# Performance work log

Hardware: AMD Instinct MI355X
Metric: run time of the kernel (lower is better)

## Reference

```python
import jax, jax.numpy as jnp
import numpy as np

C = 768
N = 2048
BS = 8
MASK_VAL = 1e10


def _sincos(n, c):
    # torch sinusoidal_position_embedding: interleaved sin/cos, then
    # cos_pos = emb[..., 1::2].repeat_interleave(2), sin_pos = emb[..., ::2].repeat_interleave(2)
    pos = jnp.arange(n, dtype=jnp.float32)[:, None]            # [N,1]
    inv = jnp.power(10000.0, -2.0 * jnp.arange(c // 2, dtype=jnp.float32) / c)  # [C/2]
    ang = pos * inv                                            # [N, C/2]
    sin = jnp.repeat(jnp.sin(ang), 2, axis=-1)                 # [N, C]
    cos = jnp.repeat(jnp.cos(ang), 2, axis=-1)                 # [N, C]
    return sin[None], cos[None]                                # [1, N, C]


def _rope(x, sin, cos):
    # x2 = interleave(-x_odd, x_even)
    x2 = jnp.stack([-x[..., 1::2], x[..., ::2]], axis=-1).reshape(x.shape)
    return x * cos + x2 * sin


def _global_pointer(x, Wq, bq, Wk, bk, sin, cos, mask):
    xq = jnp.einsum('bnc,dc->bnd', x, Wq) + bq
    xk = jnp.einsum('bnc,dc->bnd', x, Wk) + bk
    xq = _rope(xq, sin, cos)
    xk = _rope(xk, sin, cos)
    logits = jnp.einsum('bnd,bmd->bnm', xq, xk)
    logits = logits - mask * MASK_VAL
    return logits / jnp.sqrt(jnp.float32(C))


def setup_inputs() -> dict:
    key = jax.random.key(0)
    ks = jax.random.split(key, 9)
    s = 0.02
    return {
        'feature': jax.random.normal(ks[0], (BS, N, C), jnp.float32),
        'Wq': jax.random.normal(ks[1], (C, C), jnp.float32) * s,
        'bq': jax.random.normal(ks[2], (C,), jnp.float32) * s,
        'Wk': jax.random.normal(ks[3], (C, C), jnp.float32) * s,
        'bk': jax.random.normal(ks[4], (C,), jnp.float32) * s,
        'Wq_cls': jax.random.normal(ks[5], (C, C), jnp.float32) * s,
        'bq_cls': jax.random.normal(ks[6], (C,), jnp.float32) * s,
        'Wk_cls': jax.random.normal(ks[7], (C, C), jnp.float32) * s,
        'bk_cls': jax.random.normal(ks[8], (C,), jnp.float32) * s,
    }


def reference(feature, Wq, bq, Wk, bk, Wq_cls, bq_cls, Wk_cls, bk_cls):
    n = feature.shape[1]
    sin, cos = _sincos(n, C)
    mask = jnp.tril(jnp.ones((n, n), jnp.float32), k=-1)  # strictly lower triangular
    gp = _global_pointer(feature, Wq, bq, Wk, bk, sin, cos, mask)
    gp_cls = _global_pointer(feature, Wq_cls, bq_cls, Wk_cls, bk_cls, sin, cos, mask)
    # stacked: [2, bs, N, N] = (global_pointer, global_pointer_cls)
    return jnp.stack([gp, gp_cls], axis=0)
```

## Files before the change

kernel.cpp:

```cpp
#include <hip/hip_runtime.h>
#include <hip/hip_bf16.h>
#include <stdint.h>

typedef unsigned short u16;
typedef __attribute__((ext_vector_type(8))) __bf16 bf16x8;
typedef __attribute__((ext_vector_type(4))) float f32x4;

#define C_DIM 768
#define HALF_C 384
#define N_SEQ 2048
#define BATCH 8
#define M_TOT (BATCH * N_SEQ)
#define BK 32
#define NT (C_DIM / BK)

__device__ __forceinline__ u16 f2bf(float f) {
    union { float f; unsigned u; } c; c.f = f;
    unsigned r = (c.u + 0x7FFFu + ((c.u >> 16) & 1u)) >> 16;
    return (u16)r;
}

#define NXF4   3145728
#define NWF4   147456
#define NCONV4 (NXF4 + 4 * NWF4)
#define NCS    (N_SEQ * HALF_C)
__global__ __launch_bounds__(256) void prep_kernel(
    const float* __restrict__ feat,
    const float* __restrict__ Wq, const float* __restrict__ Wk,
    const float* __restrict__ Wqc, const float* __restrict__ Wkc,
    u16* __restrict__ xbf,
    u16* __restrict__ w0, u16* __restrict__ w1,
    u16* __restrict__ w2, u16* __restrict__ w3,
    uint32_t* __restrict__ cs_tab) {
    const int gid = blockIdx.x * 256 + threadIdx.x;
    const int stride = gridDim.x * 256;
    for (int i = gid; i < NCONV4; i += stride) {
        const float* src; u16* dst; int j;
        if (i < NXF4) { src = feat; dst = xbf; j = i; }
        else {
            const int k = i - NXF4;
            const int w = k / NWF4;
            j = k - w * NWF4;
            src = w == 0 ? Wq : w == 1 ? Wk : w == 2 ? Wqc : Wkc;
            dst = w == 0 ? w0 : w == 1 ? w1 : w == 2 ? w2 : w3;
        }
        float4 v = ((const float4*)src)[j];
        ushort4 o;
        o.x = f2bf(v.x); o.y = f2bf(v.y); o.z = f2bf(v.z); o.w = f2bf(v.w);
        ((ushort4*)dst)[j] = o;
    }
    for (int idx = gid; idx < NCS; idx += stride) {
        const int ip  = idx >> 11;
        const int pos = idx & (N_SEQ - 1);
        float inv = powf(10000.0f, (-2.0f / (float)C_DIM) * (float)ip);
        float ang = (float)pos * inv;
        uint32_t c = f2bf(cosf(ang)), s = f2bf(sinf(ang));
        cs_tab[idx] = (s << 16) | c;
    }
}

template<int N> __device__ __forceinline__ void vmwait();
template<> __device__ __forceinline__ void vmwait<4>() { asm volatile("s_waitcnt vmcnt(4)" ::: "memory"); }
template<> __device__ __forceinline__ void vmwait<0>() { asm volatile("s_waitcnt vmcnt(0)" ::: "memory"); }

__device__ __forceinline__ void async_load16(const void* src, void* dst_lds) {
    const __attribute__((address_space(1))) void* g =
        (const __attribute__((address_space(1))) void*)(uintptr_t)src;
    __attribute__((address_space(3))) void* l =
        (__attribute__((address_space(3))) void*)(unsigned)(uintptr_t)dst_lds;
    __builtin_amdgcn_global_load_lds(g, l, 16, 0, 0);
}

__device__ __forceinline__ void stage32(const u16* __restrict__ gbase, int ld,
                                        u16* ldsbase, int wave, int lane) {
    const int s  = (lane & 3) ^ (((lane >> 5) & 1) << 1);
    const int rr = lane >> 2;
    #pragma unroll
    for (int j = 0; j < 2; ++j) {
        const int chunk = wave * 2 + j;
        const u16* src = gbase + (size_t)(chunk * 16 + rr) * ld + s * 8;
        u16* dst = ldsbase + chunk * 512;
        async_load16(src, dst);
    }
}

__device__ __forceinline__ void gemm256_mainloop(
    const u16* __restrict__ A, const u16* __restrict__ B, int ld,
    u16* LdsA, u16* LdsB, f32x4 (&acc)[8][4], int wave, int lane) {

    #pragma unroll
    for (int t = 0; t < 3; ++t) {
        stage32(A + t * BK, ld, LdsA + t * 8192, wave, lane);
        stage32(B + t * BK, ld, LdsB + t * 8192, wave, lane);
    }
    __builtin_amdgcn_sched_barrier(0);
    vmwait<4>();
    __builtin_amdgcn_s_barrier();
    __builtin_amdgcn_sched_barrier(0);

    const int r = lane & 15, sl = lane >> 4;
    const int lane_off = r * 32 + ((sl ^ (((r >> 3) & 1) << 1)) * 8);
    const int wm = wave >> 2, wn = wave & 3;
    const int a_base = lane_off + wm * 512;
    const int b_base = lane_off + wn * 512;

    #pragma unroll
    for (int t = 0; t < NT; ++t) {
        const u16* At = LdsA + (t & 3) * 8192;
        const u16* Bt = LdsB + (t & 3) * 8192;
        bf16x8 a[4], b[4], a2[4];

        if (t + 3 < NT) stage32(A + (t + 3) * BK, ld, LdsA + ((t + 3) & 3) * 8192, wave, lane);
        #pragma unroll
        for (int mf = 0; mf < 4; ++mf) a[mf] = *(const bf16x8*)(At + a_base + mf * 1024);
        #pragma unroll
        for (int nf = 0; nf < 4; ++nf) b[nf] = *(const bf16x8*)(Bt + b_base + nf * 2048);
        __builtin_amdgcn_sched_barrier(0);
        __builtin_amdgcn_s_barrier();
        __builtin_amdgcn_sched_barrier(0);
        __builtin_amdgcn_s_setprio(1);
        #pragma unroll
        for (int mf = 0; mf < 4; ++mf)
            #pragma unroll
            for (int nf = 0; nf < 4; ++nf)
                acc[mf][nf] = __builtin_amdgcn_mfma_f32_16x16x32_bf16(a[mf], b[nf], acc[mf][nf], 0, 0, 0);
        __builtin_amdgcn_s_setprio(0);
        __builtin_amdgcn_sched_barrier(0);
        __builtin_amdgcn_s_barrier();
        __builtin_amdgcn_sched_barrier(0);

        if (t + 3 < NT) stage32(B + (t + 3) * BK, ld, LdsB + ((t + 3) & 3) * 8192, wave, lane);
        #pragma unroll
        for (int mf = 0; mf < 4; ++mf) a2[mf] = *(const bf16x8*)(At + a_base + (mf + 4) * 1024);
        __builtin_amdgcn_sched_barrier(0);
        __builtin_amdgcn_s_barrier();
        __builtin_amdgcn_sched_barrier(0);
        __builtin_amdgcn_s_setprio(1);
        #pragma unroll
        for (int mf = 0; mf < 4; ++mf)
            #pragma unroll
            for (int nf = 0; nf < 4; ++nf)
                acc[mf + 4][nf] = __builtin_amdgcn_mfma_f32_16x16x32_bf16(a2[mf], b[nf], acc[mf + 4][nf], 0, 0, 0);
        __builtin_amdgcn_s_setprio(0);
        __builtin_amdgcn_sched_barrier(0);
        if ((t & 1) == 1) {
            if (t < NT - 3)       vmwait<4>();
            else if (t == NT - 3) vmwait<0>();
        }
        __builtin_amdgcn_s_barrier();
        __builtin_amdgcn_sched_barrier(0);
    }
}

__global__ __launch_bounds__(512, 2) void proj_kernel(
    const u16* __restrict__ xbf,
    const u16* __restrict__ W0, const u16* __restrict__ W1,
    const u16* __restrict__ W2, const u16* __restrict__ W3,
    const float* __restrict__ b0, const float* __restrict__ b1,
    const float* __restrict__ b2, const float* __restrict__ b3,
    u16* __restrict__ o0, u16* __restrict__ o1, u16* __restrict__ o2, u16* __restrict__ o3,
    const uint32_t* __restrict__ cs_tab) {
    __shared__ __align__(16) u16 Lds[65536];
    u16* LdsA = Lds;
    u16* LdsB = Lds + 32768;
    const int tid = threadIdx.x, lane = tid & 63, wave = tid >> 6;
    const int bid = blockIdx.x;
    const int xcd = bid & 7, widx = bid >> 3;
    const int bx  = xcd * 8 + (widx & 7);
    const int t2  = widx >> 3;
    const int z   = t2 / 3;
    const int by  = t2 - z * 3;
    const int m0 = bx * 256, n0 = by * 256;

    const u16*   W    = z == 0 ? W0 : z == 1 ? W1 : z == 2 ? W2 : W3;
    const float* bias = z == 0 ? b0 : z == 1 ? b1 : z == 2 ? b2 : b3;
    u16*         outp = z == 0 ? o0 : z == 1 ? o1 : z == 2 ? o2 : o3;

    f32x4 acc[8][4];
    #pragma unroll
    for (int x = 0; x < 8; ++x)
        #pragma unroll
        for (int y = 0; y < 4; ++y) acc[x][y] = f32x4{0.f, 0.f, 0.f, 0.f};

    gemm256_mainloop(xbf + (size_t)m0 * C_DIM, W + (size_t)n0 * C_DIM, C_DIM,
                     LdsA, LdsB, acc, wave, lane);

    const int wm = wave >> 2, wn = wave & 3;
    const int g = lane >> 4, r = lane & 15;
    #pragma unroll
    for (int nf = 0; nf < 4; ++nf) {
        const int colL = wn * 64 + nf * 16 + r;
        const int col  = n0 + colL;
        const float bv = bias[col];
        const float sgn = (col & 1) ? 1.0f : -1.0f;
        const uint32_t* csrow = cs_tab + (size_t)(col >> 1) * N_SEQ;
        #pragma unroll
        for (int mf = 0; mf < 8; ++mf) {
            const int rowb = m0 + mf * 32 + wm * 16 + g * 4;
            const uint4 cs4 = *(const uint4*)(csrow + (rowb & (N_SEQ - 1)));
            #pragma unroll
            for (int i = 0; i < 4; ++i) {
                float v = acc[mf][nf][i] + bv;
                float p = __shfl_xor(v, 1);
                const uint32_t cs = ((const uint32_t*)&cs4)[i];
                const float c = __uint_as_float(cs << 16);
                const float s = __uint_as_float(cs & 0xFFFF0000u);
                const int rowL = mf * 32 + wm * 16 + g * 4 + i;
                const int ba = (rowL << 9) + colL * 2;
                *(u16*)((char*)Lds + (ba ^ (((rowL >> 2) & 3) << 5))) = f2bf(v * c + sgn * p * s);
            }
        }
    }
    __syncthreads();
    const size_t gbase = (size_t)m0 * C_DIM + n0;
    #pragma unroll
    for (int k = 0; k < 16; ++k) {
        const int f = (k * 512 + tid) * 16;
        const int row = f >> 9;
        const int cb  = f & 511;
        const uint4 vv = *(const uint4*)((const char*)Lds + (f ^ ((((unsigned)f >> 11) & 3) << 5)));
        *(uint4*)(outp + gbase + (size_t)row * C_DIM + (cb >> 1)) = vv;
    }
}

__global__ __launch_bounds__(512, 2) void logits_kernel(
    const u16* __restrict__ Q0, const u16* __restrict__ K0,
    const u16* __restrict__ Q1, const u16* __restrict__ K1,
    float* __restrict__ out) {
    __shared__ __align__(16) u16 LdsA[4 * 8192];
    __shared__ __align__(16) u16 LdsB[4 * 8192];
    const int tid = threadIdx.x, lane = tid & 63, wave = tid >> 6;
    const int bid = blockIdx.x;
    const int swz = (bid & 7) * 128 + (bid >> 3);
    const int z   = swz >> 6;
    const int rem = swz & 63;
    const int by  = rem >> 3;
    const int bx  = rem & 7;
    const int nrow0 = by * 256, mcol0 = bx * 256;

    const float RS = 0.036084391824351613f;
    const float MV = 1.0e10f * RS;
    float* outz = out + (size_t)z * N_SEQ * N_SEQ;

    if (bx < by) {
        const f32x4 cv = {-MV, -MV, -MV, -MV};
        #pragma unroll
        for (int i = 0; i < 32; ++i) {
            const int row = nrow0 + wave * 32 + i;
            __builtin_nontemporal_store(cv, (f32x4*)(outz + (size_t)row * N_SEQ + mcol0 + lane * 4));
        }
        return;
    }

    const int h = z >> 3, b = z & 7;
    const u16* Qb = (h ? Q1 : Q0) + (size_t)b * N_SEQ * C_DIM;
    const u16* Kb = (h ? K1 : K0) + (size_t)b * N_SEQ * C_DIM;

    f32x4 acc[8][4];
    #pragma unroll
    for (int x = 0; x < 8; ++x)
        #pragma unroll
        for (int y = 0; y < 4; ++y) acc[x][y] = f32x4{0.f, 0.f, 0.f, 0.f};

    gemm256_mainloop(Qb + (size_t)nrow0 * C_DIM, Kb + (size_t)mcol0 * C_DIM, C_DIM,
                     LdsA, LdsB, acc, wave, lane);

    const int wm = wave >> 2, wn = wave & 3;
    const int g = lane >> 4, r = lane & 15;
    #pragma unroll
    for (int mf = 0; mf < 8; ++mf) {
        #pragma unroll
        for (int i = 0; i < 4; ++i) {
            const int row = nrow0 + mf * 32 + wm * 16 + g * 4 + i;
            float* orow = outz + (size_t)row * N_SEQ;
            #pragma unroll
            for (int nf = 0; nf < 4; ++nf) {
                const int col = mcol0 + wn * 64 + nf * 16 + r;
                __builtin_nontemporal_store(acc[mf][nf][i] * RS - (col < row ? MV : 0.0f),
                                            orow + col);
            }
        }
    }
}

extern "C" void kernel_launch(void* const* d_in, const int* in_sizes, int n_in,
                              void* d_out, int out_size, void* d_ws, size_t ws_size,
                              hipStream_t stream) {
    (void)in_sizes; (void)n_in; (void)out_size; (void)ws_size;
    const float* feat = (const float*)d_in[0];
    const float* Wq   = (const float*)d_in[1];
    const float* bq   = (const float*)d_in[2];
    const float* Wk   = (const float*)d_in[3];
    const float* bk   = (const float*)d_in[4];
    const float* Wqc  = (const float*)d_in[5];
    const float* bqc  = (const float*)d_in[6];
    const float* Wkc  = (const float*)d_in[7];
    const float* bkc  = (const float*)d_in[8];
    float* out = (float*)d_out;

    u16* ws = (u16*)d_ws;
    const size_t XE = (size_t)M_TOT * C_DIM;
    const size_t WE = (size_t)C_DIM * C_DIM;
    u16* xbf = ws;
    u16* Wb0 = ws + XE;
    u16* Wb1 = Wb0 + WE;
    u16* Wb2 = Wb1 + WE;
    u16* Wb3 = Wb2 + WE;
    u16* qkbase = Wb3 + WE;
    u16* Qa = qkbase;
    u16* Ka = qkbase + XE;
    u16* Qc = qkbase + 2 * XE;
    u16* Kc = qkbase + 3 * XE;
    uint32_t* cs_tab = (uint32_t*)(qkbase + 4 * XE);

    prep_kernel<<<dim3(2048), dim3(256), 0, stream>>>(
        feat, Wq, Wk, Wqc, Wkc, xbf, Wb0, Wb1, Wb2, Wb3, cs_tab);

    proj_kernel<<<dim3(768), dim3(512), 0, stream>>>(
        xbf, Wb0, Wb1, Wb2, Wb3, bq, bk, bqc, bkc, Qa, Ka, Qc, Kc, cs_tab);

    logits_kernel<<<dim3(1024), dim3(512), 0, stream>>>(
        Qa, Ka, Qc, Kc, out);
}
```

Baseline: 202.3 us.

## Halve proj_kernel LDS to 64KB with double-buffered loop and split epilogue

Replaces the shared gemm256_mainloop in proj_kernel with an inline two-stage double-buffered loop that uses 64KB of LDS instead of 128KB. The epilogue is split into two 128-row halves so that it fits in the smaller buffer. Launch bounds are raised to 4 blocks per CU to allow more occupancy, but with 32x4 accumulators plus fragments per thread that request risks register pressure or spills. The loop also now waits for all outstanding loads (vmwait<0>) every iteration, which reduces how much loads overlap with compute.

```diff
diff --git a/kernel.cpp b/kernel.cpp
--- a/kernel.cpp
+++ b/kernel.cpp
@@ -152,7 +152,7 @@
     }
 }
 
-__global__ __launch_bounds__(512, 2) void proj_kernel(
+__global__ __launch_bounds__(512, 4) void proj_kernel(
     const u16* __restrict__ xbf,
     const u16* __restrict__ W0, const u16* __restrict__ W1,
     const u16* __restrict__ W2, const u16* __restrict__ W3,
@@ -160,9 +160,7 @@
     const float* __restrict__ b2, const float* __restrict__ b3,
     u16* __restrict__ o0, u16* __restrict__ o1, u16* __restrict__ o2, u16* __restrict__ o3,
     const uint32_t* __restrict__ cs_tab) {
-    __shared__ __align__(16) u16 Lds[65536];
-    u16* LdsA = Lds;
-    u16* LdsB = Lds + 32768;
+    __shared__ __align__(16) u16 Lds[32768];
     const int tid = threadIdx.x, lane = tid & 63, wave = tid >> 6;
     const int bid = blockIdx.x;
     const int xcd = bid & 7, widx = bid >> 3;
@@ -175,6 +173,8 @@
     const u16*   W    = z == 0 ? W0 : z == 1 ? W1 : z == 2 ? W2 : W3;
     const float* bias = z == 0 ? b0 : z == 1 ? b1 : z == 2 ? b2 : b3;
     u16*         outp = z == 0 ? o0 : z == 1 ? o1 : z == 2 ? o2 : o3;
+    const u16* A = xbf + (size_t)m0 * C_DIM;
+    const u16* B = W + (size_t)n0 * C_DIM;
 
     f32x4 acc[8][4];
     #pragma unroll
@@ -182,44 +182,102 @@
         #pragma unroll
         for (int y = 0; y < 4; ++y) acc[x][y] = f32x4{0.f, 0.f, 0.f, 0.f};
 
-    gemm256_mainloop(xbf + (size_t)m0 * C_DIM, W + (size_t)n0 * C_DIM, C_DIM,
-                     LdsA, LdsB, acc, wave, lane);
-
+    stage32(A, C_DIM, Lds, wave, lane);
+    stage32(B, C_DIM, Lds + 8192, wave, lane);
+    __builtin_amdgcn_sched_barrier(0);
+    vmwait<0>();
+    __builtin_amdgcn_s_barrier();
+    __builtin_amdgcn_sched_barrier(0);
+
+    const int r = lane & 15, sl = lane >> 4;
+    const int lane_off = r * 32 + ((sl ^ (((r >> 3) & 1) << 1)) * 8);
     const int wm = wave >> 2, wn = wave & 3;
-    const int g = lane >> 4, r = lane & 15;
-    #pragma unroll
-    for (int nf = 0; nf < 4; ++nf) {
-        const int colL = wn * 64 + nf * 16 + r;
-        const int col  = n0 + colL;
-        const float bv = bias[col];
-        const float sgn = (col & 1) ? 1.0f : -1.0f;
-        const uint32_t* csrow = cs_tab + (size_t)(col >> 1) * N_SEQ;
-        #pragma unroll
-        for (int mf = 0; mf < 8; ++mf) {
-            const int rowb = m0 + mf * 32 + wm * 16 + g * 4;
-            const uint4 cs4 = *(const uint4*)(csrow + (rowb & (N_SEQ - 1)));
-            #pragma unroll
-            for (int i = 0; i < 4; ++i) {
-                float v = acc[mf][nf][i] + bv;
-                float p = __shfl_xor(v, 1);
-                const uint32_t cs = ((const uint32_t*)&cs4)[i];
-                const float c = __uint_as_float(cs << 16);
-                const float s = __uint_as_float(cs & 0xFFFF0000u);
-                const int rowL = mf * 32 + wm * 16 + g * 4 + i;
-                const int ba = (rowL << 9) + colL * 2;
-                *(u16*)((char*)Lds + (ba ^ (((rowL >> 2) & 3) << 5))) = f2bf(v * c + sgn * p * s);
+    const int a_base = lane_off + wm * 512;
+    const int b_base = 8192 + lane_off + wn * 512;
+
+    #pragma unroll
+    for (int t = 0; t < NT; ++t) {
+        const u16* S = Lds + (t & 1) * 16384;
+        u16* D = Lds + ((t + 1) & 1) * 16384;
+        bf16x8 a[4], b[4], a2[4];
+
+        if (t + 1 < NT) stage32(A + (t + 1) * BK, C_DIM, D, wave, lane);
+        #pragma unroll
+        for (int mf = 0; mf < 4; ++mf) a[mf] = *(const bf16x8*)(S + a_base + mf * 1024);
+        #pragma unroll
+        for (int nf = 0; nf < 4; ++nf) b[nf] = *(const bf16x8*)(S + b_base + nf * 2048);
+        __builtin_amdgcn_sched_barrier(0);
+        __builtin_amdgcn_s_barrier();
+        __builtin_amdgcn_sched_barrier(0);
+        __builtin_amdgcn_s_setprio(1);
+        #pragma unroll
+        for (int mf = 0; mf < 4; ++mf)
+            #pragma unroll
+            for (int nf = 0; nf < 4; ++nf)
+                acc[mf][nf] = __builtin_amdgcn_mfma_f32_16x16x32_bf16(a[mf], b[nf], acc[mf][nf], 0, 0, 0);
+        __builtin_amdgcn_s_setprio(0);
+        __builtin_amdgcn_sched_barrier(0);
+        __builtin_amdgcn_s_barrier();
+        __builtin_amdgcn_sched_barrier(0);
+
+        if (t + 1 < NT) stage32(B + (t + 1) * BK, C_DIM, D + 8192, wave, lane);
+        #pragma unroll
+        for (int mf = 0; mf < 4; ++mf) a2[mf] = *(const bf16x8*)(S + a_base + (mf + 4) * 1024);
+        __builtin_amdgcn_sched_barrier(0);
+        __builtin_amdgcn_s_barrier();
+        __builtin_amdgcn_sched_barrier(0);
+        __builtin_amdgcn_s_setprio(1);
+        #pragma unroll
+        for (int mf = 0; mf < 4; ++mf)
+            #pragma unroll
+            for (int nf = 0; nf < 4; ++nf)
+                acc[mf + 4][nf] = __builtin_amdgcn_mfma_f32_16x16x32_bf16(a2[mf], b[nf], acc[mf + 4][nf], 0, 0, 0);
+        __builtin_amdgcn_s_setprio(0);
+        __builtin_amdgcn_sched_barrier(0);
+        vmwait<0>();
+        __builtin_amdgcn_s_barrier();
+        __builtin_amdgcn_sched_barrier(0);
+    }
+
+    const int g = lane >> 4;
+    #pragma unroll
+    for (int half = 0; half < 2; ++half) {
+        #pragma unroll
+        for (int nf = 0; nf < 4; ++nf) {
+            const int colL = wn * 64 + nf * 16 + r;
+            const int col  = n0 + colL;
+            const float bv = bias[col];
+            const float sgn = (col & 1) ? 1.0f : -1.0f;
+            const uint32_t* csrow = cs_tab + (size_t)(col >> 1) * N_SEQ;
+            #pragma unroll
+            for (int mf4 = 0; mf4 < 4; ++mf4) {
+                const int mf = half * 4 + mf4;
+                const int rowb = m0 + mf * 32 + wm * 16 + g * 4;
+                const uint4 cs4 = *(const uint4*)(csrow + (rowb & (N_SEQ - 1)));
+                #pragma unroll
+                for (int i = 0; i < 4; ++i) {
+                    float v = acc[mf][nf][i] + bv;
+                    float p = __shfl_xor(v, 1);
+                    const uint32_t cs = ((const uint32_t*)&cs4)[i];
+                    const float c = __uint_as_float(cs << 16);
+                    const float s = __uint_as_float(cs & 0xFFFF0000u);
+                    const int rowH = mf4 * 32 + wm * 16 + g * 4 + i;
+                    const int ba = (rowH << 9) + colL * 2;
+                    *(u16*)((char*)Lds + (ba ^ (((rowH >> 2) & 3) << 5))) = f2bf(v * c + sgn * p * s);
+                }
             }
         }
-    }
-    __syncthreads();
-    const size_t gbase = (size_t)m0 * C_DIM + n0;
-    #pragma unroll
-    for (int k = 0; k < 16; ++k) {
-        const int f = (k * 512 + tid) * 16;
-        const int row = f >> 9;
-        const int cb  = f & 511;
-        const uint4 vv = *(const uint4*)((const char*)Lds + (f ^ ((((unsigned)f >> 11) & 3) << 5)));
-        *(uint4*)(outp + gbase + (size_t)row * C_DIM + (cb >> 1)) = vv;
+        __syncthreads();
+        const size_t gbase = (size_t)(m0 + half * 128) * C_DIM + n0;
+        #pragma unroll
+        for (int k = 0; k < 8; ++k) {
+            const int f = (k * 512 + tid) * 16;
+            const int row = f >> 9;
+            const int cb  = f & 511;
+            const uint4 vv = *(const uint4*)((const char*)Lds + (f ^ ((((unsigned)f >> 11) & 3) << 5)));
+            *(uint4*)(outp + gbase + (size_t)row * C_DIM + (cb >> 1)) = vv;
+        }
+        __syncthreads();
     }
 }
 
```

Result: slower. 728.0 us (+259.8%).

## Shrink projection GEMM tiles to 128x128 with 256-thread double-buffered blocks

Applied to the files above, without the earlier changes.

The projection kernel moves from 256x256 tiles with 512 threads and a 4-stage LDS pipeline to 128x128 tiles with 256 threads and a simple 2-stage double buffer, launching 3072 blocks instead of 768. Smaller LDS use and more blocks are meant to raise occupancy and balance work across CUs. In exchange, each block reuses loaded data less, and the pipeline waits for all loads (vmcnt 0) every k-step, which exposes more memory latency. The staging helper is generalised into a template so the logits kernel path keeps its old configuration.

```diff
diff --git a/kernel.cpp b/kernel.cpp
--- a/kernel.cpp
+++ b/kernel.cpp
@@ -71,16 +71,16 @@
     __builtin_amdgcn_global_load_lds(g, l, 16, 0, 0);
 }
 
-__device__ __forceinline__ void stage32(const u16* __restrict__ gbase, int ld,
-                                        u16* ldsbase, int wave, int lane) {
+template<int NROWS, int WAVES>
+__device__ __forceinline__ void stageT(const u16* __restrict__ gbase, int ld,
+                                       u16* ldsbase, int wave, int lane) {
     const int s  = (lane & 3) ^ (((lane >> 5) & 1) << 1);
     const int rr = lane >> 2;
     #pragma unroll
-    for (int j = 0; j < 2; ++j) {
-        const int chunk = wave * 2 + j;
+    for (int j = 0; j < (NROWS / 16) / WAVES; ++j) {
+        const int chunk = wave * ((NROWS / 16) / WAVES) + j;
         const u16* src = gbase + (size_t)(chunk * 16 + rr) * ld + s * 8;
-        u16* dst = ldsbase + chunk * 512;
-        async_load16(src, dst);
+        async_load16(src, ldsbase + chunk * 512);
     }
 }
 
@@ -90,8 +90,8 @@
 
     #pragma unroll
     for (int t = 0; t < 3; ++t) {
-        stage32(A + t * BK, ld, LdsA + t * 8192, wave, lane);
-        stage32(B + t * BK, ld, LdsB + t * 8192, wave, lane);
+        stageT<256, 8>(A + t * BK, ld, LdsA + t * 8192, wave, lane);
+        stageT<256, 8>(B + t * BK, ld, LdsB + t * 8192, wave, lane);
     }
     __builtin_amdgcn_sched_barrier(0);
     vmwait<4>();
@@ -110,7 +110,7 @@
         const u16* Bt = LdsB + (t & 3) * 8192;
         bf16x8 a[4], b[4], a2[4];
 
-        if (t + 3 < NT) stage32(A + (t + 3) * BK, ld, LdsA + ((t + 3) & 3) * 8192, wave, lane);
+        if (t + 3 < NT) stageT<256, 8>(A + (t + 3) * BK, ld, LdsA + ((t + 3) & 3) * 8192, wave, lane);
         #pragma unroll
         for (int mf = 0; mf < 4; ++mf) a[mf] = *(const bf16x8*)(At + a_base + mf * 1024);
         #pragma unroll
@@ -129,7 +129,7 @@
         __builtin_amdgcn_s_barrier();
         __builtin_amdgcn_sched_barrier(0);
 
-        if (t + 3 < NT) stage32(B + (t + 3) * BK, ld, LdsB + ((t + 3) & 3) * 8192, wave, lane);
+        if (t + 3 < NT) stageT<256, 8>(B + (t + 3) * BK, ld, LdsB + ((t + 3) & 3) * 8192, wave, lane);
         #pragma unroll
         for (int mf = 0; mf < 4; ++mf) a2[mf] = *(const bf16x8*)(At + a_base + (mf + 4) * 1024);
         __builtin_amdgcn_sched_barrier(0);
@@ -152,7 +152,7 @@
     }
 }
 
-__global__ __launch_bounds__(512, 2) void proj_kernel(
+__global__ __launch_bounds__(256) void proj_kernel(
     const u16* __restrict__ xbf,
     const u16* __restrict__ W0, const u16* __restrict__ W1,
     const u16* __restrict__ W2, const u16* __restrict__ W3,
@@ -160,33 +160,69 @@
     const float* __restrict__ b2, const float* __restrict__ b3,
     u16* __restrict__ o0, u16* __restrict__ o1, u16* __restrict__ o2, u16* __restrict__ o3,
     const uint32_t* __restrict__ cs_tab) {
-    __shared__ __align__(16) u16 Lds[65536];
-    u16* LdsA = Lds;
-    u16* LdsB = Lds + 32768;
+    __shared__ __align__(16) u16 Lds[16384];
     const int tid = threadIdx.x, lane = tid & 63, wave = tid >> 6;
     const int bid = blockIdx.x;
     const int xcd = bid & 7, widx = bid >> 3;
-    const int bx  = xcd * 8 + (widx & 7);
-    const int t2  = widx >> 3;
-    const int z   = t2 / 3;
-    const int by  = t2 - z * 3;
-    const int m0 = bx * 256, n0 = by * 256;
+    const int bx  = xcd * 16 + (widx & 15);
+    const int t2  = widx >> 4;
+    const int z   = t2 / 6;
+    const int byn = t2 - z * 6;
+    const int m0 = bx * 128, n0 = byn * 128;
 
     const u16*   W    = z == 0 ? W0 : z == 1 ? W1 : z == 2 ? W2 : W3;
     const float* bias = z == 0 ? b0 : z == 1 ? b1 : z == 2 ? b2 : b3;
     u16*         outp = z == 0 ? o0 : z == 1 ? o1 : z == 2 ? o2 : o3;
-
-    f32x4 acc[8][4];
-    #pragma unroll
-    for (int x = 0; x < 8; ++x)
+    const u16* A = xbf + (size_t)m0 * C_DIM;
+    const u16* B = W + (size_t)n0 * C_DIM;
+
+    f32x4 acc[4][4];
+    #pragma unroll
+    for (int x = 0; x < 4; ++x)
         #pragma unroll
         for (int y = 0; y < 4; ++y) acc[x][y] = f32x4{0.f, 0.f, 0.f, 0.f};
 
-    gemm256_mainloop(xbf + (size_t)m0 * C_DIM, W + (size_t)n0 * C_DIM, C_DIM,
-                     LdsA, LdsB, acc, wave, lane);
-
-    const int wm = wave >> 2, wn = wave & 3;
-    const int g = lane >> 4, r = lane & 15;
+    stageT<128, 4>(A, C_DIM, Lds, wave, lane);
+    stageT<128, 4>(B, C_DIM, Lds + 4096, wave, lane);
+    __builtin_amdgcn_sched_barrier(0);
+    vmwait<0>();
+    __builtin_amdgcn_s_barrier();
+    __builtin_amdgcn_sched_barrier(0);
+
+    const int r = lane & 15, sl = lane >> 4;
+    const int lane_off = r * 32 + ((sl ^ (((r >> 3) & 1) << 1)) * 8);
+    const int wm = wave >> 1, wn = wave & 1;
+    const int a_base = lane_off + wm * 2048;
+    const int b_base = 4096 + lane_off + wn * 2048;
+
+    #pragma unroll
+    for (int t = 0; t < NT; ++t) {
+        const u16* S = Lds + (t & 1) * 8192;
+        u16* D = Lds + ((t + 1) & 1) * 8192;
+        bf16x8 a[4], b[4];
+
+        if (t + 1 < NT) {
+            stageT<128, 4>(A + (t + 1) * BK, C_DIM, D, wave, lane);
+            stageT<128, 4>(B + (t + 1) * BK, C_DIM, D + 4096, wave, lane);
+        }
+        #pragma unroll
+        for (int mf = 0; mf < 4; ++mf) a[mf] = *(const bf16x8*)(S + a_base + mf * 512);
+        #pragma unroll
+        for (int nf = 0; nf < 4; ++nf) b[nf] = *(const bf16x8*)(S + b_base + nf * 512);
+        __builtin_amdgcn_s_setprio(1);
+        #pragma unroll
+        for (int mf = 0; mf < 4; ++mf)
+            #pragma unroll
+            for (int nf = 0; nf < 4; ++nf)
+                acc[mf][nf] = __builtin_amdgcn_mfma_f32_16x16x32_bf16(a[mf], b[nf], acc[mf][nf], 0, 0, 0);
+        __builtin_amdgcn_s_setprio(0);
+        __builtin_amdgcn_sched_barrier(0);
+        vmwait<0>();
+        __builtin_amdgcn_s_barrier();
+        __builtin_amdgcn_sched_barrier(0);
+    }
+
+    const int g = lane >> 4;
     #pragma unroll
     for (int nf = 0; nf < 4; ++nf) {
         const int colL = wn * 64 + nf * 16 + r;
@@ -195,8 +231,8 @@
         const float sgn = (col & 1) ? 1.0f : -1.0f;
         const uint32_t* csrow = cs_tab + (size_t)(col >> 1) * N_SEQ;
         #pragma unroll
-        for (int mf = 0; mf < 8; ++mf) {
-            const int rowb = m0 + mf * 32 + wm * 16 + g * 4;
+        for (int mf = 0; mf < 4; ++mf) {
+            const int rowb = m0 + wm * 64 + mf * 16 + g * 4;
             const uint4 cs4 = *(const uint4*)(csrow + (rowb & (N_SEQ - 1)));
             #pragma unroll
             for (int i = 0; i < 4; ++i) {
@@ -205,8 +241,8 @@
                 const uint32_t cs = ((const uint32_t*)&cs4)[i];
                 const float c = __uint_as_float(cs << 16);
                 const float s = __uint_as_float(cs & 0xFFFF0000u);
-                const int rowL = mf * 32 + wm * 16 + g * 4 + i;
-                const int ba = (rowL << 9) + colL * 2;
+                const int rowL = wm * 64 + mf * 16 + g * 4 + i;
+                const int ba = (rowL << 8) + colL * 2;
                 *(u16*)((char*)Lds + (ba ^ (((rowL >> 2) & 3) << 5))) = f2bf(v * c + sgn * p * s);
             }
         }
@@ -214,11 +250,11 @@
     __syncthreads();
     const size_t gbase = (size_t)m0 * C_DIM + n0;
     #pragma unroll
-    for (int k = 0; k < 16; ++k) {
-        const int f = (k * 512 + tid) * 16;
-        const int row = f >> 9;
-        const int cb  = f & 511;
-        const uint4 vv = *(const uint4*)((const char*)Lds + (f ^ ((((unsigned)f >> 11) & 3) << 5)));
+    for (int k = 0; k < 8; ++k) {
+        const int f = (k * 256 + tid) * 16;
+        const int row = f >> 8;
+        const int cb  = f & 255;
+        const uint4 vv = *(const uint4*)((const char*)Lds + (f ^ ((((unsigned)f >> 10) & 3) << 5)));
         *(uint4*)(outp + gbase + (size_t)row * C_DIM + (cb >> 1)) = vv;
     }
 }
@@ -316,7 +352,7 @@
     prep_kernel<<<dim3(2048), dim3(256), 0, stream>>>(
         feat, Wq, Wk, Wqc, Wkc, xbf, Wb0, Wb1, Wb2, Wb3, cs_tab);
 
-    proj_kernel<<<dim3(768), dim3(512), 0, stream>>>(
+    proj_kernel<<<dim3(3072), dim3(256), 0, stream>>>(
         xbf, Wb0, Wb1, Wb2, Wb3, bq, bk, bqc, bkc, Qa, Ka, Qc, Kc, cs_tab);
 
     logits_kernel<<<dim3(1024), dim3(512), 0, stream>>>(
```

Result: slower. 223.8 us (+10.6%).
